# Performance work log

Measured on AMD Instinct MI355X. Metric: run time of the kernel, lower is better.

## Reference

```python
import jax, jax.numpy as jnp
import numpy as np

NUM_HEADS = 12

def setup_inputs() -> dict:
    key = jax.random.key(0)
    k1, k2, k3 = jax.random.split(key, 3)
    B, T, H = 2, 2048, 768
    x = jax.random.normal(k1, (B, T, H), dtype=jnp.float32)
    attn_mask = jnp.ones((B, T), dtype=jnp.int32)
    Wqkv = jax.random.normal(k2, (H, 3 * H), dtype=jnp.float32) * 0.02
    bqkv = jnp.zeros((3 * H,), dtype=jnp.float32)
    Wproj = jax.random.normal(k3, (H, H), dtype=jnp.float32) * 0.02
    bproj = jnp.zeros((H,), dtype=jnp.float32)
    return {"x": x, "attn_mask": attn_mask, "Wqkv": Wqkv, "bqkv": bqkv,
            "Wproj": Wproj, "bproj": bproj}

def reference(x, attn_mask, Wqkv, bqkv, Wproj, bproj):
    B, T, H = x.shape
    nh = NUM_HEADS
    hd = H // nh
    qkv = x @ Wqkv + bqkv                      # [B,T,3H]
    q, k, v = jnp.split(qkv, 3, axis=-1)
    # [B,T,H] -> [B,nh,T,hd]
    def heads(t):
        return t.reshape(B, T, nh, hd).transpose(0, 2, 1, 3)
    q, k, v = heads(q), heads(k), heads(v)
    scores = jnp.einsum('bhqd,bhkd->bhqk', q, k) / jnp.sqrt(jnp.float32(hd))
    causal = jnp.tril(jnp.ones((T, T), dtype=bool))          # allowed positions
    key_ok = attn_mask.astype(bool)[:, None, None, :]        # [B,1,1,T]
    allowed = causal[None, None] & key_ok
    scores = jnp.where(allowed, scores, -jnp.inf)
    weights = jax.nn.softmax(scores, axis=-1)                # dropout=0 (eval)
    out = jnp.einsum('bhqk,bhkd->bhqd', weights, v)
    out = out.transpose(0, 2, 1, 3).reshape(B, T, H)
    return out @ Wproj + bproj
```

## Files before the change

### kernel.cpp

```cpp
#include <hip/hip_runtime.h>
#include <stdint.h>

typedef unsigned short u16;
typedef unsigned int   u32;
typedef unsigned char  u8;
typedef __attribute__((ext_vector_type(8))) short short8;
typedef __attribute__((ext_vector_type(4))) float f32x4;
typedef __attribute__((ext_vector_type(4))) unsigned short u16x4;
typedef __attribute__((ext_vector_type(4))) unsigned int u32x4;

#define DEV static __device__ __forceinline__

static constexpr int Bc = 2, Tc = 2048, Hc = 768, NH = 12, HD = 64;
static constexpr int BTc = Bc * Tc;
static constexpr int N3 = 3 * Hc;
static constexpr int NBH = Bc * NH;
static constexpr int NITEMS = 32 * NBH;
static constexpr float QSCALE = 0.125f * 1.44269504088896f;
static constexpr float MRINIT = -1.0e38f;
static constexpr float SMASK  = -3.0e38f;

DEV u16 f2bf(float f) {
  u32 u = __float_as_uint(f);
  u32 r = (u + 0x7fffu + ((u >> 16) & 1u)) >> 16;
  return (u16)r;
}

DEV float fexp2(float x) {
#if __has_builtin(__builtin_amdgcn_exp2f)
  return __builtin_amdgcn_exp2f(x);
#else
  return exp2f(x);
#endif
}

DEV u32 cvtpk_bf16(float lo, float hi) {
  u32 r;
  asm("v_cvt_pk_bf16_f32 %0, %1, %2" : "=v"(r) : "v"(lo), "v"(hi));
  return r;
}

DEV void gl_lds16(const u16* g, u16* l) {
  __builtin_amdgcn_global_load_lds(
      (const __attribute__((address_space(1))) u32*)g,
      (__attribute__((address_space(3))) u32*)l, 16, 0, 0);
}

#define MFMA(a, b, c) __builtin_amdgcn_mfma_f32_16x16x32_bf16((a), (b), (c), 0, 0, 0)

__global__ void k_cvt(const float4* __restrict__ in, uint4* __restrict__ out, int n8,
                      const int* __restrict__ mask, u8* __restrict__ flags,
                      u32* __restrict__ ctr) {
  if (blockIdx.x == 0 && threadIdx.x < 64) {
    int t = threadIdx.x;
    if (t == 0) *ctr = 0;
    int b = t >> 5, kb = t & 31;
    const int* m = mask + b * Tc + kb * 64;
    int all = 1;
    for (int i = 0; i < 64; ++i) all &= (m[i] != 0);
    flags[b * 32 + kb] = (u8)all;
  }
  int i = blockIdx.x * 256 + threadIdx.x;
  if (i >= n8) return;
  float4 a = in[2 * i], b = in[2 * i + 1];
  uint4 o;
  o.x = f2bf(a.x) | ((u32)f2bf(a.y) << 16);
  o.y = f2bf(a.z) | ((u32)f2bf(a.w) << 16);
  o.z = f2bf(b.x) | ((u32)f2bf(b.y) << 16);
  o.w = f2bf(b.z) | ((u32)f2bf(b.w) << 16);
  out[i] = o;
}

__global__ __launch_bounds__(256) void k_transpose_w2(const float* __restrict__ Wqkv,
                                                      const float* __restrict__ Wproj,
                                                      u16* __restrict__ WqkvT,
                                                      u16* __restrict__ WprojT) {
  __shared__ u16 tile[64][65];
  int y = blockIdx.y, x = blockIdx.x;
  const float* in; u16* out; int R, C, r0, c0;
  if (y < 12) { in = Wqkv; out = WqkvT; R = Hc; C = N3; r0 = y * 64; c0 = x * 64; }
  else {
    if (x >= 12) return;
    in = Wproj; out = WprojT; R = Hc; C = Hc; r0 = (y - 12) * 64; c0 = x * 64;
  }
  int tx = threadIdx.x, ty = threadIdx.y;
  for (int i = ty; i < 64; i += 4)
    tile[i][tx] = f2bf(in[(size_t)(r0 + i) * C + c0 + tx]);
  __syncthreads();
  for (int i = ty; i < 64; i += 4)
    out[(size_t)(c0 + i) * R + r0 + tx] = tile[tx][i];
}

template <int EPI>
__global__ __launch_bounds__(256) void k_gemm(const u16* __restrict__ A,
                                              const u16* __restrict__ BTm,
                                              const float* __restrict__ bias,
                                              u16* __restrict__ oQ, u16* __restrict__ oK,
                                              u16* __restrict__ oV, float* __restrict__ oF,
                                              int M, int N, int K) {
  __shared__ u16 As[128 * 32];
  __shared__ u16 Bs[128 * 32];
  const int tid = threadIdx.x;
  const int lane = tid & 63, wave = tid >> 6;
  const int wr = wave >> 1, wc = wave & 1;
  const int row0 = blockIdx.y * 128, col0 = blockIdx.x * 128;

  f32x4 acc[4][4];
#pragma unroll
  for (int m = 0; m < 4; ++m)
#pragma unroll
    for (int n = 0; n < 4; ++n) acc[m][n] = (f32x4)(0.f);

  const int srow = lane >> 2;
  const int sg = lane & 3;
  const int sf = (lane >> 3) & 3;
  const int kfetch = ((sg ^ sf) * 8);

  const int r16 = lane & 15;
  const int g = lane >> 4;
  const int fr = (r16 >> 1) & 3;
  const int koff = ((g ^ fr) * 8);

  for (int k0 = 0; k0 < K; k0 += 32) {
    if (k0) __syncthreads();
#pragma unroll
    for (int p = 0; p < 2; ++p) {
      int seg = wave * 2 + p;
      int row = seg * 16 + srow;
      gl_lds16(A + (size_t)(row0 + row) * K + k0 + kfetch, &As[seg * 512 + lane * 8]);
      gl_lds16(BTm + (size_t)(col0 + row) * K + k0 + kfetch, &Bs[seg * 512 + lane * 8]);
    }
    __syncthreads();
    short8 af[4], bf[4];
#pragma unroll
    for (int m = 0; m < 4; ++m)
      af[m] = *(const short8*)&As[(wr * 64 + m * 16 + r16) * 32 + koff];
#pragma unroll
    for (int n = 0; n < 4; ++n)
      bf[n] = *(const short8*)&Bs[(wc * 64 + n * 16 + r16) * 32 + koff];
#pragma unroll
    for (int m = 0; m < 4; ++m)
#pragma unroll
      for (int n = 0; n < 4; ++n)
        acc[m][n] = MFMA(af[m], bf[n], acc[m][n]);
  }

#pragma unroll
  for (int m = 0; m < 4; ++m) {
    int rowg = row0 + wr * 64 + m * 16 + g * 4;
#pragma unroll
    for (int n = 0; n < 4; ++n) {
      int colg = col0 + wc * 64 + n * 16 + r16;
      float bv = bias[colg];
      if constexpr (EPI == 0) {
        int which = colg / Hc;
        int hc = colg - which * Hc;
        int h = hc >> 6, d = hc & 63;
        int b = rowg >> 11, t0 = rowg & 2047;
        if (which == 2) {
          int o = t0 & 31;
          int t0p = (t0 & ~31) | (((o >> 2) & 3) * 8 + ((o >> 4) & 1) * 4);
          u16x4 pk;
#pragma unroll
          for (int r = 0; r < 4; ++r) pk[r] = f2bf(acc[m][n][r] + bv);
          *(u16x4*)&oV[((size_t)(b * NH + h) * HD + d) * Tc + t0p] = pk;
        } else {
#pragma unroll
          for (int r = 0; r < 4; ++r) {
            float v = acc[m][n][r] + bv;
            size_t dst = ((size_t)(b * NH + h) * Tc + t0 + r) * HD + d;
            if (which == 0) oQ[dst] = f2bf(v * QSCALE);
            else            oK[dst] = f2bf(v);
          }
        }
      } else {
#pragma unroll
        for (int r = 0; r < 4; ++r)
          oF[(size_t)(rowg + r) * Hc + colg] = acc[m][n][r] + bv;
      }
    }
  }
}

__global__ __launch_bounds__(512, 4) void k_attn(const u16* __restrict__ Qh,
                                                 const u16* __restrict__ Kh,
                                                 const u16* __restrict__ VT,
                                                 const int* __restrict__ mask,
                                                 const u8* __restrict__ flags,
                                                 u16* __restrict__ O,
                                                 u32* __restrict__ ctr) {
  __shared__ u16 Ks[4][4096];
  __shared__ u16 Vs[4][4096];
  __shared__ float mlb[128];
  __shared__ int s_item;
  const int tid = threadIdx.x, lane = tid & 63, wave = tid >> 6;
  const int qgrp = wave >> 1;
  const int kh = wave & 1;
  const int r16 = lane & 15, g = lane >> 4;
  const int r7 = r16 & 7;
  const int skey = lane >> 3;
  const int sgr = lane & 7;
  const int sgd = ((sgr ^ skey) * 8);

  const int off0 = r16 * 64 + ((g ^ r7) * 8);
  const int off1 = r16 * 64 + (((4 + g) ^ r7) * 8);
  const int offv = kh ? off1 : off0;

  for (;;) {
    if (tid == 0) s_item = (int)atomicAdd(ctr, 1u);
    __syncthreads();
    const int item = s_item;
    if (item >= NITEMS) break;
    const int qt = 31 - item / NBH;
    const int bh = item % NBH;
    const int b = bh / NH, h = bh - b * NH;
    const int q0 = qt * 64;
    const int nt = qt + 1;
    const int qg = q0 + qgrp * 16 + r16;
    const int* mrow = mask + b * Tc;
    const u8* frow = flags + b * 32;

    const u16* qbase = Qh + ((size_t)bh * Tc + qg) * HD;
    const short8 qf0 = *(const short8*)(qbase + g * 8);
    const short8 qf1 = *(const short8*)(qbase + 32 + g * 8);

    f32x4 acc[4];
#pragma unroll
    for (int n = 0; n < 4; ++n) acc[n] = (f32x4)(0.f);
    float mrun = MRINIT, lrun = 0.f;

    const u16* kgb = Kh + (size_t)bh * Tc * HD;
    const u16* vgb = VT + (size_t)bh * HD * Tc;

    auto stage = [&](int slot, int kb) {
      int rloc = wave * 8 + skey;
      gl_lds16(kgb + (size_t)(kb + rloc) * HD + sgd, &Ks[slot][wave * 512 + lane * 8]);
      gl_lds16(vgb + (size_t)rloc * Tc + kb + sgd, &Vs[slot][wave * 512 + lane * 8]);
    };

    f32x4 sP0, sP1;
    auto process = [&](int u, f32x4 s0, f32x4 s1) {
      const int kbw = 64 * u + 32 * kh;
      const bool diag = (u == nt - 1);
      if (diag || !frow[u]) {
        const int fl = frow[u];
#pragma unroll
        for (int np = 0; np < 2; ++np)
#pragma unroll
          for (int r = 0; r < 4; ++r) {
            int keyg = kbw + 16 * np + 4 * g + r;
            bool ok = fl ? true : (mrow[keyg] != 0);
            if (diag) ok = ok && (keyg <= qg);
            if (!ok) { if (np == 0) s0[r] = SMASK; else s1[r] = SMASK; }
          }
      }
      float lm = fmaxf(fmaxf(fmaxf(s0[0], s0[1]), fmaxf(s0[2], s0[3])),
                       fmaxf(fmaxf(s1[0], s1[1]), fmaxf(s1[2], s1[3])));
      if (!__all(lm <= mrun + 8.0f)) {
        float rm = fmaxf(lm, __shfl_xor(lm, 16));
        rm = fmaxf(rm, __shfl_xor(rm, 32));
        float nm = fmaxf(mrun, rm);
        float alpha = fexp2(mrun - nm);
        mrun = nm;
        lrun *= alpha;
#pragma unroll
        for (int r = 0; r < 4; ++r) {
          float ar = __shfl(alpha, g * 4 + r);
          acc[0][r] *= ar; acc[1][r] *= ar; acc[2][r] *= ar; acc[3][r] *= ar;
        }
      }
      float p0[4], p1[4];
#pragma unroll
      for (int r = 0; r < 4; ++r) {
        p0[r] = fexp2(s0[r] - mrun);
        p1[r] = fexp2(s1[r] - mrun);
      }
      lrun += ((p0[0] + p0[1]) + (p0[2] + p0[3])) + ((p1[0] + p1[1]) + (p1[2] + p1[3]));
      u32x4 PL;
      PL[0] = cvtpk_bf16(p0[0], p0[1]); PL[1] = cvtpk_bf16(p0[2], p0[3]);
      PL[2] = cvtpk_bf16(p1[0], p1[1]); PL[3] = cvtpk_bf16(p1[2], p1[3]);
      short8 pa = __builtin_bit_cast(short8, PL);
      const u16* Vc = &Vs[u & 3][0];
      __builtin_amdgcn_s_setprio(1);
#pragma unroll
      for (int n = 0; n < 4; ++n) {
        short8 vf = *(const short8*)&Vc[n * 1024 + offv];
        acc[n] = MFMA(pa, vf, acc[n]);
      }
      __builtin_amdgcn_s_setprio(0);
    };

    stage(0, 0);
    if (nt > 1) stage(1, 64);

    for (int t = 0; t < nt; ++t) {
      const int kb = t * 64;
      const int rem = nt - 1 - t;

      if (rem >= 1) asm volatile("s_waitcnt vmcnt(2)" ::: "memory");
      else          asm volatile("s_waitcnt vmcnt(0)" ::: "memory");
      __builtin_amdgcn_sched_barrier(0);
      __builtin_amdgcn_s_barrier();
      __builtin_amdgcn_sched_barrier(0);

      if (rem >= 2) stage((t + 2) & 3, kb + 128);

      const u16* Kc = &Ks[t & 3][0];
      f32x4 sN0, sN1;
      __builtin_amdgcn_s_setprio(1);
      {
        const int ng = 2 * kh;
        short8 kf0 = *(const short8*)&Kc[ng * 1024 + off0];
        short8 kf1 = *(const short8*)&Kc[ng * 1024 + off1];
        f32x4 z = (f32x4)(0.f);
        z = MFMA(kf0, qf0, z); z = MFMA(kf1, qf1, z);
        sN0 = z;
        short8 kf2 = *(const short8*)&Kc[(ng + 1) * 1024 + off0];
        short8 kf3 = *(const short8*)&Kc[(ng + 1) * 1024 + off1];
        f32x4 w = (f32x4)(0.f);
        w = MFMA(kf2, qf0, w); w = MFMA(kf3, qf1, w);
        sN1 = w;
      }
      __builtin_amdgcn_s_setprio(0);

      if (t > 0) process(t - 1, sP0, sP1);
      sP0 = sN0; sP1 = sN1;
    }
    process(nt - 1, sP0, sP1);

    float lt = lrun + __shfl_xor(lrun, 16);
    lt += __shfl_xor(lt, 32);

    __syncthreads();
    float* ab = (float*)&Ks[0][0] + qgrp * 1024;
    if (kh == 1) {
#pragma unroll
      for (int n = 0; n < 4; ++n)
#pragma unroll
        for (int r = 0; r < 4; ++r)
          ab[(4 * g + r) * 64 + 16 * n + r16] = acc[n][r];
      if (g == 0) {
        mlb[qgrp * 32 + r16 * 2]     = mrun;
        mlb[qgrp * 32 + r16 * 2 + 1] = lt;
      }
    }
    __syncthreads();
    if (kh == 0) {
#pragma unroll
      for (int r = 0; r < 4; ++r) {
        int q = 4 * g + r;
        float mA = __shfl(mrun, q);
        float lA = __shfl(lt, q);
        float mB = mlb[qgrp * 32 + q * 2];
        float lB = mlb[qgrp * 32 + q * 2 + 1];
        float ms = fmaxf(mA, mB);
        float cA = fexp2(mA - ms);
        float cB = fexp2(mB - ms);
        float linv = 1.0f / (lA * cA + lB * cB);
        int qr = q0 + qgrp * 16 + q;
        u16* orow = O + ((size_t)(b * Tc + qr)) * Hc + h * 64;
#pragma unroll
        for (int n = 0; n < 4; ++n) {
          float v = (acc[n][r] * cA + ab[q * 64 + 16 * n + r16] * cB) * linv;
          orow[n * 16 + r16] = f2bf(v);
        }
      }
    }
  }
}

extern "C" void kernel_launch(void* const* d_in, const int* in_sizes, int n_in,
                              void* d_out, int out_size, void* d_ws, size_t ws_size,
                              hipStream_t stream) {
  const float* x = (const float*)d_in[0];
  const int* mask = (const int*)d_in[1];
  const float* Wqkv = (const float*)d_in[2];
  const float* bqkv = (const float*)d_in[3];
  const float* Wproj = (const float*)d_in[4];
  const float* bproj = (const float*)d_in[5];
  float* out = (float*)d_out;

  char* ws = (char*)d_ws;
  size_t off = 0;
  auto alloc = [&](size_t bytes) {
    char* p = ws + off;
    off += (bytes + 255) & ~(size_t)255;
    return p;
  };
  u16* xb     = (u16*)alloc((size_t)BTc * Hc * 2);
  u16* WqkvT  = (u16*)alloc((size_t)N3 * Hc * 2);
  u16* WprojT = (u16*)alloc((size_t)Hc * Hc * 2);
  u16* Qh     = (u16*)alloc((size_t)BTc * Hc * 2);
  u16* Kh     = (u16*)alloc((size_t)BTc * Hc * 2);
  u16* VT     = (u16*)alloc((size_t)BTc * Hc * 2);
  u32* ctr    = (u32*)alloc(256);
  u8*  flags  = (u8*)alloc(256);
  u16* Ob     = xb;

  int n8 = BTc * Hc / 8;
  k_cvt<<<(n8 + 255) / 256, 256, 0, stream>>>((const float4*)x, (uint4*)xb, n8,
                                              mask, flags, ctr);
  k_transpose_w2<<<dim3(36, 24), dim3(64, 4), 0, stream>>>(Wqkv, Wproj, WqkvT, WprojT);
  k_gemm<0><<<dim3(N3 / 128, BTc / 128), 256, 0, stream>>>(xb, WqkvT, bqkv, Qh, Kh, VT,
                                                           nullptr, BTc, N3, Hc);
  k_attn<<<dim3(512), 512, 0, stream>>>(Qh, Kh, VT, mask, flags, Ob, ctr);
  k_gemm<1><<<dim3(Hc / 128, BTc / 128), 256, 0, stream>>>(Ob, WprojT, bproj, nullptr,
                                                           nullptr, nullptr, out, BTc, Hc, Hc);
}
```

Before: 103.6 us.

## Triple-buffer GEMM LDS loads, XCD-swizzle GEMM tiles, per-XCD attention work queues

The GEMM kernel now keeps three LDS stages with async global-to-LDS loads issued two iterations ahead. Partial vmcnt waits and a single barrier per k-step replace the load-then-sync loop, so memory latency can overlap the MFMA work. GEMM workgroup IDs are remapped so consecutive tiles land on the same XCD for better L2 reuse. The attention kernel's single atomic work counter is split into eight per-XCD counters, each serving three (batch, head) pairs, which keeps K/V reuse in each XCD's L2. The trade-offs are more LDS per GEMM block, possibly lower occupancy, and a fixed 3-heads-per-XCD partition that can leave XCDs unevenly loaded.

After: 102.0 us. About the same (-1.6%).

```diff
diff --git a/kernel.cpp b/kernel.cpp
--- a/kernel.cpp
+++ b/kernel.cpp
@@ -15,7 +15,7 @@
 static constexpr int BTc = Bc * Tc;
 static constexpr int N3 = 3 * Hc;
 static constexpr int NBH = Bc * NH;
-static constexpr int NITEMS = 32 * NBH;
+static constexpr int IPX = 96;
 static constexpr float QSCALE = 0.125f * 1.44269504088896f;
 static constexpr float MRINIT = -1.0e38f;
 static constexpr float SMASK  = -3.0e38f;
@@ -53,7 +53,7 @@
                       u32* __restrict__ ctr) {
   if (blockIdx.x == 0 && threadIdx.x < 64) {
     int t = threadIdx.x;
-    if (t == 0) *ctr = 0;
+    if (t < 8) ctr[t] = 0;
     int b = t >> 5, kb = t & 31;
     const int* m = mask + b * Tc + kb * 64;
     int all = 1;
@@ -98,12 +98,17 @@
                                               u16* __restrict__ oQ, u16* __restrict__ oK,
                                               u16* __restrict__ oV, float* __restrict__ oF,
                                               int M, int N, int K) {
-  __shared__ u16 As[128 * 32];
-  __shared__ u16 Bs[128 * 32];
+  __shared__ u16 As[3][4096];
+  __shared__ u16 Bs[3][4096];
   const int tid = threadIdx.x;
   const int lane = tid & 63, wave = tid >> 6;
   const int wr = wave >> 1, wc = wave & 1;
-  const int row0 = blockIdx.y * 128, col0 = blockIdx.x * 128;
+
+  const int gx = gridDim.x;
+  const int nwg = gx * gridDim.y;
+  const int lin = blockIdx.y * gx + blockIdx.x;
+  const int wg = (lin & 7) * (nwg >> 3) + (lin >> 3);
+  const int row0 = (wg / gx) * 128, col0 = (wg % gx) * 128;
 
   f32x4 acc[4][4];
 #pragma unroll
@@ -121,23 +126,37 @@
   const int fr = (r16 >> 1) & 3;
   const int koff = ((g ^ fr) * 8);
 
-  for (int k0 = 0; k0 < K; k0 += 32) {
-    if (k0) __syncthreads();
+  auto stageG = [&](int slot, int k0) {
 #pragma unroll
     for (int p = 0; p < 2; ++p) {
       int seg = wave * 2 + p;
       int row = seg * 16 + srow;
-      gl_lds16(A + (size_t)(row0 + row) * K + k0 + kfetch, &As[seg * 512 + lane * 8]);
-      gl_lds16(BTm + (size_t)(col0 + row) * K + k0 + kfetch, &Bs[seg * 512 + lane * 8]);
+      gl_lds16(A + (size_t)(row0 + row) * K + k0 + kfetch, &As[slot][seg * 512 + lane * 8]);
+      gl_lds16(BTm + (size_t)(col0 + row) * K + k0 + kfetch, &Bs[slot][seg * 512 + lane * 8]);
     }
-    __syncthreads();
+  };
+
+  const int nk = K >> 5;
+  stageG(0, 0);
+  if (nk > 1) stageG(1, 32);
+
+  for (int kt = 0; kt < nk; ++kt) {
+    if (kt + 1 < nk) asm volatile("s_waitcnt vmcnt(4)" ::: "memory");
+    else             asm volatile("s_waitcnt vmcnt(0)" ::: "memory");
+    __builtin_amdgcn_sched_barrier(0);
+    __builtin_amdgcn_s_barrier();
+    __builtin_amdgcn_sched_barrier(0);
+    if (kt + 2 < nk) stageG((kt + 2) % 3, (kt + 2) * 32);
+
+    const u16* Ac = &As[kt % 3][0];
+    const u16* Bcur = &Bs[kt % 3][0];
     short8 af[4], bf[4];
 #pragma unroll
     for (int m = 0; m < 4; ++m)
-      af[m] = *(const short8*)&As[(wr * 64 + m * 16 + r16) * 32 + koff];
+      af[m] = *(const short8*)&Ac[(wr * 64 + m * 16 + r16) * 32 + koff];
 #pragma unroll
     for (int n = 0; n < 4; ++n)
-      bf[n] = *(const short8*)&Bs[(wc * 64 + n * 16 + r16) * 32 + koff];
+      bf[n] = *(const short8*)&Bcur[(wc * 64 + n * 16 + r16) * 32 + koff];
 #pragma unroll
     for (int m = 0; m < 4; ++m)
 #pragma unroll
@@ -206,13 +225,15 @@
   const int off1 = r16 * 64 + (((4 + g) ^ r7) * 8);
   const int offv = kh ? off1 : off0;
 
+  const int xcd = blockIdx.x & 7;
+
   for (;;) {
-    if (tid == 0) s_item = (int)atomicAdd(ctr, 1u);
+    if (tid == 0) s_item = (int)atomicAdd(ctr + xcd, 1u);
     __syncthreads();
     const int item = s_item;
-    if (item >= NITEMS) break;
-    const int qt = 31 - item / NBH;
-    const int bh = item % NBH;
+    if (item >= IPX) break;
+    const int qt = 31 - item / 3;
+    const int bh = xcd * 3 + item % 3;
     const int b = bh / NH, h = bh - b * NH;
     const int q0 = qt * 64;
     const int nt = qt + 1;
```
